# Performance work log

Measured on AMD Instinct MI355X. Metric: run time of the kernel, lower is better.

Reference implementation:

```python
import jax, jax.numpy as jnp
import numpy as np

B, T, IN, H = 1024, 200, 128, 128

def _linear_params(key, out_dim, in_dim):
    kw, kb = jax.random.split(key)
    bound = 1.0 / np.sqrt(in_dim)
    w = jax.random.uniform(kw, (out_dim, in_dim), jnp.float32, -bound, bound)
    b = jax.random.uniform(kb, (out_dim,), jnp.float32, -bound, bound)
    return w, b

def setup_inputs() -> dict:
    key = jax.random.key(0)
    ks = jax.random.split(key, 10)
    targets = jax.random.normal(ks[0], (B, T, IN), jnp.float32)
    history_states = jax.random.normal(ks[1], (B, T, H), jnp.float32)
    W_w, W_b = _linear_params(ks[2], H, IN)
    xu_w, xu_b = _linear_params(ks[3], H, H)
    hu_w, hu_b = _linear_params(ks[4], H, H)
    xr_w, xr_b = _linear_params(ks[5], H, H)
    hr_w, hr_b = _linear_params(ks[6], H, H)
    xg_w, xg_b = _linear_params(ks[7], H, H)
    hg_w, hg_b = _linear_params(ks[8], H, H)
    ln2_w, ln2_b = _linear_params(ks[9], H, IN + H)
    return dict(targets=targets, history_states=history_states,
                W_w=W_w, W_b=W_b, xu_w=xu_w, xu_b=xu_b, hu_w=hu_w, hu_b=hu_b,
                xr_w=xr_w, xr_b=xr_b, hr_w=hr_w, hr_b=hr_b,
                xg_w=xg_w, xg_b=xg_b, hg_w=hg_w, hg_b=hg_b,
                ln2_w=ln2_w, ln2_b=ln2_b)

def reference(targets, history_states, W_w, W_b, xu_w, xu_b, hu_w, hu_b,
              xr_w, xr_b, hr_w, hr_b, xg_w, xg_b, hg_w, hg_b, ln2_w, ln2_b):
    # attention weights: softmax over time of <W(targets), history>
    aw = jnp.einsum('bti,hi->bth', targets, W_w) + W_b            # [B,T,H]
    att = jax.nn.softmax(jnp.sum(aw * history_states, -1, keepdims=True), axis=1)  # [B,T,1]

    # precompute input-side projections as big GEMMs (same math as per-step Linear)
    xu = jnp.einsum('bth,oh->bto', history_states, xu_w) + xu_b   # [B,T,H]
    xr = jnp.einsum('bth,oh->bto', history_states, xr_w) + xr_b
    xg = jnp.einsum('bth,oh->bto', history_states, xg_w) + xg_b

    def step(h, xs):
        xu_t, xr_t, xg_t, a_t = xs                                 # [B,H],[B,H],[B,H],[B,1]
        u = jax.nn.sigmoid(xu_t + h @ hu_w.T + hu_b) * a_t
        r = jax.nn.sigmoid(xr_t + h @ hr_w.T + hr_b)
        g = jnp.tanh(xg_t + r * (h @ hg_w.T + hg_b))
        h = (1.0 - u) * h + u * g
        return h, None

    h0 = jnp.zeros((targets.shape[0], hu_w.shape[0]), targets.dtype)
    # scan over time: move T to leading axis
    xs = (jnp.swapaxes(xu, 0, 1), jnp.swapaxes(xr, 0, 1),
          jnp.swapaxes(xg, 0, 1), jnp.swapaxes(att, 0, 1))
    h, _ = jax.lax.scan(step, h0, xs)

    out = jnp.concatenate([h, targets[:, 0]], axis=-1) @ ln2_w.T + ln2_b
    return out
```

## Files before the change

kernel.cpp:

```cpp
#include <hip/hip_runtime.h>

#define B_ 1024
#define T_ 200
#define H_ 128
#define TSTR (T_ + 4)

typedef __attribute__((ext_vector_type(8))) short short8;
typedef __attribute__((ext_vector_type(4))) float f32x4;

#define MFMA(a, b, c) __builtin_amdgcn_mfma_f32_16x16x32_bf16((a), (b), (c), 0, 0, 0)

static __device__ __forceinline__ short f2bf(float f) {
  unsigned u = __float_as_uint(f);
  u += 0x7fffu + ((u >> 16) & 1u);
  return (short)(u >> 16);
}
static __device__ __forceinline__ float bf2f(short s) {
  return __uint_as_float(((unsigned)(unsigned short)s) << 16);
}
static __device__ __forceinline__ unsigned pack2bf_rne(float a, float b) {
  unsigned ua = __float_as_uint(a);
  ua += 0x7fffu + ((ua >> 16) & 1u);
  unsigned ub = __float_as_uint(b);
  ub += 0x7fffu + ((ub >> 16) & 1u);
  return (ua >> 16) | (ub & 0xFFFF0000u);
}
static __device__ __forceinline__ unsigned pack2bf_trunc(float a, float b) {
  return (__float_as_uint(a) >> 16) | (__float_as_uint(b) & 0xFFFF0000u);
}
static __device__ __forceinline__ float rcp_f(float x) { return __builtin_amdgcn_rcpf(x); }
static __device__ __forceinline__ float exp2_f(float x) { return __builtin_amdgcn_exp2f(x); }
static __device__ __forceinline__ void ck_barrier() {
  asm volatile("s_waitcnt lgkmcnt(0)\n\ts_barrier" ::: "memory");
}

__global__ __launch_bounds__(512, 1) void proj_scores_kernel(
    const float* __restrict__ tgt, const float* __restrict__ hist,
    const float* __restrict__ Ww, const float* __restrict__ Wb,
    float* __restrict__ scores, short* __restrict__ histbf) {
  const int tc = blockIdx.x, bb = blockIdx.y;
  const int nt = (tc == 12) ? 8 : 16;
  const int t0 = tc * 16;
  const int tid = threadIdx.x;
  const int lane = tid & 63, w = tid >> 6;
  const int n = lane & 15, q = lane >> 4;

  __shared__ short tgt_hi[2][16 * 128];
  __shared__ short tgt_lo[2][16 * 128];
  __shared__ float hist_f[2][16 * 132];
  __shared__ float sp[2][16 * 8];

  short8 whi[4], wlo[4];
  f32x4 wb4;
  {
    const int o = w * 16 + n;
#pragma unroll
    for (int ks = 0; ks < 4; ++ks) {
      const float* p = Ww + o * H_ + ks * 32 + q * 8;
      short8 h, l;
#pragma unroll
      for (int j = 0; j < 8; ++j) {
        float f = p[j];
        short hv = f2bf(f);
        h[j] = hv;
        l[j] = f2bf(f - bf2f(hv));
      }
      whi[ks] = h;
      wlo[ks] = l;
    }
    wb4 = *(const f32x4*)(Wb + w * 16 + q * 4);
  }

  const int sm = tid >> 5, cs = tid & 31;
  const int g = cs >> 1, half = cs & 1;
  const int spos16 = sm * 128 + ((g ^ (sm & 7)) * 8) + half * 4;
  const int sposf = sm * 132 + cs * 4;
  const size_t rowbase = ((size_t)(bb * 16 + sm) * T_) * H_ + cs * 4;

  const int cu = tid;
  const int cks = cu >> 7, crem = cu & 127, cwl = crem >> 1, chalf = crem & 1;
  const int crow = cwl & 15, ckb = cks * 32 + (cwl >> 4) * 8 + chalf * 4;

  float4 hv = *(const float4*)(hist + rowbase + (size_t)t0 * H_);
  float4 tv = *(const float4*)(tgt + rowbase + (size_t)t0 * H_);
  {
    *(float4*)&hist_f[0][sposf] = hv;
    uint2 hi, lo;
    hi.x = pack2bf_rne(tv.x, tv.y);
    hi.y = pack2bf_rne(tv.z, tv.w);
    lo.x = pack2bf_rne(tv.x - bf2f((short)(hi.x)), tv.y - bf2f((short)(hi.x >> 16)));
    lo.y = pack2bf_rne(tv.z - bf2f((short)(hi.y)), tv.w - bf2f((short)(hi.y >> 16)));
    *(uint2*)&tgt_hi[0][spos16] = hi;
    *(uint2*)&tgt_lo[0][spos16] = lo;
  }
  ck_barrier();

  for (int tl = 0; tl < nt; ++tl) {
    const int cur = tl & 1, nxt = cur ^ 1;
    const bool have_next = (tl + 1 < nt);
    if (have_next) {
      hv = *(const float4*)(hist + rowbase + (size_t)(t0 + tl + 1) * H_);
      tv = *(const float4*)(tgt + rowbase + (size_t)(t0 + tl + 1) * H_);
    }
    f32x4 s1 = {0, 0, 0, 0}, s2 = {0, 0, 0, 0}, s3 = {0, 0, 0, 0};
#pragma unroll
    for (int ks = 0; ks < 4; ++ks) {
      const int fp = n * 128 + ((ks * 4 + q) ^ (n & 7)) * 8;
      short8 ahi = *(short8*)&tgt_hi[cur][fp];
      short8 alo = *(short8*)&tgt_lo[cur][fp];
      s1 = MFMA(whi[ks], ahi, s1);
      s2 = MFMA(wlo[ks], ahi, s2);
      s3 = MFMA(whi[ks], alo, s3);
    }
    {
      f32x4 hv4 = *(const f32x4*)&hist_f[cur][n * 132 + w * 16 + q * 4];
      float v = (s1[0] + s2[0] + s3[0] + wb4[0]) * hv4[0];
      v += (s1[1] + s2[1] + s3[1] + wb4[1]) * hv4[1];
      v += (s1[2] + s2[2] + s3[2] + wb4[2]) * hv4[2];
      v += (s1[3] + s2[3] + s3[3] + wb4[3]) * hv4[3];
      v += __shfl_xor(v, 16);
      v += __shfl_xor(v, 32);
      if (lane < 16) sp[cur][n * 8 + w] = v;
    }
    if (histbf != nullptr) {
      const float* src = &hist_f[cur][crow * 132 + ckb];
      uint2 u;
      u.x = pack2bf_rne(src[0], src[1]);
      u.y = pack2bf_rne(src[2], src[3]);
      const size_t sb =
          (((size_t)(bb * TSTR + t0 + tl) * 4) + cks) * 512 + cwl * 8 + chalf * 4;
      *(uint2*)(histbf + sb) = u;
    }
    if (have_next) {
      *(float4*)&hist_f[nxt][sposf] = hv;
      uint2 hi, lo;
      hi.x = pack2bf_rne(tv.x, tv.y);
      hi.y = pack2bf_rne(tv.z, tv.w);
      lo.x = pack2bf_rne(tv.x - bf2f((short)(hi.x)), tv.y - bf2f((short)(hi.x >> 16)));
      lo.y = pack2bf_rne(tv.z - bf2f((short)(hi.y)), tv.w - bf2f((short)(hi.y >> 16)));
      *(uint2*)&tgt_hi[nxt][spos16] = hi;
      *(uint2*)&tgt_lo[nxt][spos16] = lo;
    }
    ck_barrier();
    if (tid < 16) {
      float s = 0.0f;
#pragma unroll
      for (int ww = 0; ww < 8; ++ww) s += sp[cur][tid * 8 + ww];
      scores[(size_t)(bb * 16 + tid) * T_ + (t0 + tl)] = s;
    }
  }
}

__global__ __launch_bounds__(256, 4) void softmax_kernel(float* __restrict__ att) {
  const int b = blockIdx.x, tid = threadIdx.x;
  const int lane = tid & 63, wave = tid >> 6;
  __shared__ float red[8];
  float v = (tid < T_) ? att[(size_t)b * T_ + tid] : -3.0e38f;
  float mx = v;
#pragma unroll
  for (int d = 1; d < 64; d <<= 1) mx = fmaxf(mx, __shfl_xor(mx, d));
  if (lane == 0) red[wave] = mx;
  __syncthreads();
  mx = fmaxf(fmaxf(red[0], red[1]), fmaxf(red[2], red[3]));
  float e = (tid < T_) ? __expf(v - mx) : 0.0f;
  float sm = e;
#pragma unroll
  for (int d = 1; d < 64; d <<= 1) sm += __shfl_xor(sm, d);
  if (lane == 0) red[4 + wave] = sm;
  __syncthreads();
  sm = red[4] + red[5] + red[6] + red[7];
  if (tid < T_) att[(size_t)b * T_ + tid] = e / sm;
}

template <bool DIRECT>
__global__ __launch_bounds__(512, 1) void scan3_kernel(
    const float* __restrict__ hist,
    const float* __restrict__ xu_w, const float* __restrict__ xu_b,
    const float* __restrict__ hu_w, const float* __restrict__ hu_b,
    const float* __restrict__ xr_w, const float* __restrict__ xr_b,
    const float* __restrict__ hr_w, const float* __restrict__ hr_b,
    const float* __restrict__ xg_w, const float* __restrict__ xg_b,
    const float* __restrict__ hg_w, const float* __restrict__ hg_b,
    const float* __restrict__ att, const short* __restrict__ histbf,
    float* __restrict__ h_out) {
  const int tid = threadIdx.x;
  const int lane = tid & 63, w = tid >> 6;
  const int n = lane & 15, q = lane >> 4;
  const int bb = blockIdx.x, r0 = bb * 16;
  const int o = w * 16 + n;
  const int ob = w * 16 + q * 4;

  constexpr float LOG2E = 1.4426950408889634f;

  __shared__ short hbuf[2][16 * 128];
  __shared__ short xbuf[2][16 * 128];

  short8 wf[6][4];
  {
    const float* Wm[6] = {xu_w, hu_w, xr_w, hr_w, xg_w, hg_w};
    const float Sc[6] = {LOG2E, LOG2E, LOG2E, LOG2E, 2.0f * LOG2E, 2.0f * LOG2E};
#pragma unroll
    for (int M = 0; M < 6; ++M)
#pragma unroll
      for (int ks = 0; ks < 4; ++ks) {
        const float* p = Wm[M] + o * H_ + ks * 32 + q * 8;
        short8 v;
#pragma unroll
        for (int j = 0; j < 8; ++j) v[j] = f2bf(p[j] * Sc[M]);
        wf[M][ks] = v;
      }
  }
  const f32x4 bu4 = (*(const f32x4*)(xu_b + ob) + *(const f32x4*)(hu_b + ob)) * LOG2E;
  const f32x4 br4 = (*(const f32x4*)(xr_b + ob) + *(const f32x4*)(hr_b + ob)) * LOG2E;
  const f32x4 bxg4 = *(const f32x4*)(xg_b + ob) * (2.0f * LOG2E);
  const f32x4 bhg4 = *(const f32x4*)(hg_b + ob) * (2.0f * LOG2E);

  for (int i = tid; i < 16 * 128; i += 512) hbuf[0][i] = 0;

  typedef union { uint4 u; short8 s; } frag_u;
  frag_u xp[2][4];
  const short* px = histbf + ((size_t)bb * TSTR * 4) * 512 + (size_t)lane * 8;
  const int sm = tid >> 5, cs = tid & 31;
  const int xpos = sm * 128 + (((cs >> 1) ^ (sm & 7)) * 8) + (cs & 1) * 4;
  const float* hrow = hist + ((size_t)(r0 + sm) * T_) * H_ + cs * 4;
  float4 xnext;

  f32x4 xq[2][3];

  if constexpr (DIRECT) {
    frag_u x0[4];
#pragma unroll
    for (int ks = 0; ks < 4; ++ks)
      x0[ks].u = *(const uint4*)(px + (size_t)(0 * 4 + ks) * 512);
#pragma unroll
    for (int ks = 0; ks < 4; ++ks)
      xp[1][ks].u = *(const uint4*)(px + (size_t)(1 * 4 + ks) * 512);
#pragma unroll
    for (int ks = 0; ks < 4; ++ks)
      xp[0][ks].u = *(const uint4*)(px + (size_t)(2 * 4 + ks) * 512);
    xq[0][0] = MFMA(wf[0][0], x0[0].s, bu4);
    xq[0][1] = MFMA(wf[2][0], x0[0].s, br4);
    xq[0][2] = MFMA(wf[4][0], x0[0].s, bxg4);
#pragma unroll
    for (int ks = 1; ks < 4; ++ks) {
      xq[0][0] = MFMA(wf[0][ks], x0[ks].s, xq[0][0]);
      xq[0][1] = MFMA(wf[2][ks], x0[ks].s, xq[0][1]);
      xq[0][2] = MFMA(wf[4][ks], x0[ks].s, xq[0][2]);
    }
  } else {
    float4 a = *(const float4*)hrow;
    uint2 u;
    u.x = pack2bf_rne(a.x, a.y);
    u.y = pack2bf_rne(a.z, a.w);
    *(uint2*)&xbuf[0][xpos] = u;
    xnext = *(const float4*)(hrow + H_);
  }

  const float* pa = att + (size_t)(r0 + n) * T_;
  f32x4 ab0 = *(const f32x4*)(pa + 0);
  f32x4 ab1 = *(const f32x4*)(pa + 4);

  float hreg[4] = {0.0f, 0.0f, 0.0f, 0.0f};
  const int wri = n * 128 + (((w * 2 + (q >> 1)) ^ (n & 7)) * 8) + (q & 1) * 4;
  ck_barrier();

  if constexpr (DIRECT) {
    const short* pxt = px + (size_t)12 * 512;
    for (int tb = 0; tb < T_; tb += 8) {
#pragma unroll
      for (int k = 0; k < 8; ++k) {
        const int t = tb + k;
        const int cur = k & 1, nxt = cur ^ 1;
        short8 ha[4];
#pragma unroll
        for (int ks = 0; ks < 4; ++ks)
          ha[ks] = *(short8*)&hbuf[cur][n * 128 + ((ks * 4 + q) ^ (n & 7)) * 8];

        f32x4 ahu = MFMA(wf[1][0], ha[0], xq[cur][0]);
        f32x4 ahr = MFMA(wf[3][0], ha[0], xq[cur][1]);
        f32x4 ahg = MFMA(wf[5][0], ha[0], bhg4);
#pragma unroll
        for (int ks = 1; ks < 4; ++ks) {
          ahu = MFMA(wf[1][ks], ha[ks], ahu);
          ahr = MFMA(wf[3][ks], ha[ks], ahr);
          ahg = MFMA(wf[5][ks], ha[ks], ahg);
        }

        {
          const short8 x0s = xp[nxt][0].s;
          xq[nxt][0] = MFMA(wf[0][0], x0s, bu4);
          xq[nxt][1] = MFMA(wf[2][0], x0s, br4);
          xq[nxt][2] = MFMA(wf[4][0], x0s, bxg4);
#pragma unroll
          for (int ks = 1; ks < 4; ++ks) {
            const short8 xs = xp[nxt][ks].s;
            xq[nxt][0] = MFMA(wf[0][ks], xs, xq[nxt][0]);
            xq[nxt][1] = MFMA(wf[2][ks], xs, xq[nxt][1]);
            xq[nxt][2] = MFMA(wf[4][ks], xs, xq[nxt][2]);
          }
        }
#pragma unroll
        for (int ks = 0; ks < 4; ++ks)
          xp[nxt][ks].u = *(const uint4*)(pxt + (size_t)(k * 4 + ks) * 512);

        const float at = ((k >> 2) & 1) ? ab1[k & 3] : ab0[k & 3];
        if (k == 3) ab0 = *(const f32x4*)(pa + ((t + 5 <= T_ - 4) ? t + 5 : T_ - 4));
        if (k == 7) ab1 = *(const f32x4*)(pa + ((t + 5 <= T_ - 4) ? t + 5 : T_ - 4));

        float hn[4];
#pragma unroll
        for (int r = 0; r < 4; ++r) {
          const float uu = at * rcp_f(1.0f + exp2_f(-ahu[r]));
          const float rr = rcp_f(1.0f + exp2_f(-ahr[r]));
          const float sg = xq[cur][2][r] + rr * ahg[r];
          const float g = 2.0f * rcp_f(1.0f + exp2_f(-sg)) - 1.0f;
          hn[r] = hreg[r] + uu * (g - hreg[r]);
          hreg[r] = hn[r];
        }

        uint2 up;
        up.x = pack2bf_trunc(hn[0], hn[1]);
        up.y = pack2bf_trunc(hn[2], hn[3]);
        *(uint2*)&hbuf[nxt][wri] = up;
        ck_barrier();
      }
      pxt += (size_t)8 * 4 * 512;
    }
  } else {
#pragma unroll 2
    for (int t = 0; t < T_; ++t) {
      const int cur = t & 1, nxt = cur ^ 1;
      short8 ha[4];
#pragma unroll
      for (int ks = 0; ks < 4; ++ks)
        ha[ks] = *(short8*)&hbuf[cur][n * 128 + ((ks * 4 + q) ^ (n & 7)) * 8];
      short8 xa[4];
#pragma unroll
      for (int ks = 0; ks < 4; ++ks)
        xa[ks] = *(short8*)&xbuf[cur][n * 128 + ((ks * 4 + q) ^ (n & 7)) * 8];
      f32x4 xu_a = MFMA(wf[0][0], xa[0], bu4);
      f32x4 xr_a = MFMA(wf[2][0], xa[0], br4);
      f32x4 xg_a = MFMA(wf[4][0], xa[0], bxg4);
#pragma unroll
      for (int ks = 1; ks < 4; ++ks) {
        xu_a = MFMA(wf[0][ks], xa[ks], xu_a);
        xr_a = MFMA(wf[2][ks], xa[ks], xr_a);
        xg_a = MFMA(wf[4][ks], xa[ks], xg_a);
      }
      f32x4 ahu = MFMA(wf[1][0], ha[0], xu_a);
      f32x4 ahr = MFMA(wf[3][0], ha[0], xr_a);
      f32x4 ahg = MFMA(wf[5][0], ha[0], bhg4);
#pragma unroll
      for (int ks = 1; ks < 4; ++ks) {
        ahu = MFMA(wf[1][ks], ha[ks], ahu);
        ahr = MFMA(wf[3][ks], ha[ks], ahr);
        ahg = MFMA(wf[5][ks], ha[ks], ahg);
      }
      const int tp = (t + 2 < T_) ? t + 2 : T_ - 1;
      const float at = ((t >> 2) & 1) ? ab1[t & 3] : ab0[t & 3];
      if ((t & 7) == 3) ab0 = *(const f32x4*)(pa + ((t + 5 <= T_ - 4) ? t + 5 : T_ - 4));
      if ((t & 7) == 7) ab1 = *(const f32x4*)(pa + ((t + 5 <= T_ - 4) ? t + 5 : T_ - 4));
      float hn[4];
#pragma unroll
      for (int r = 0; r < 4; ++r) {
        const float uu = at * rcp_f(1.0f + exp2_f(-ahu[r]));
        const float rr = rcp_f(1.0f + exp2_f(-ahr[r]));
        const float sg = xg_a[r] + rr * ahg[r];
        const float g = 2.0f * rcp_f(1.0f + exp2_f(-sg)) - 1.0f;
        hn[r] = hreg[r] + uu * (g - hreg[r]);
        hreg[r] = hn[r];
      }
      uint2 up;
      up.x = pack2bf_trunc(hn[0], hn[1]);
      up.y = pack2bf_trunc(hn[2], hn[3]);
      *(uint2*)&hbuf[nxt][wri] = up;
      uint2 u;
      u.x = pack2bf_rne(xnext.x, xnext.y);
      u.y = pack2bf_rne(xnext.z, xnext.w);
      *(uint2*)&xbuf[nxt][xpos] = u;
      xnext = *(const float4*)(hrow + (size_t)tp * H_);
      ck_barrier();
    }
  }

  f32x4 hv = {hreg[0], hreg[1], hreg[2], hreg[3]};
  *(f32x4*)(h_out + (size_t)(r0 + n) * H_ + ob) = hv;
}

__global__ __launch_bounds__(256, 4) void final_kernel(
    const float* __restrict__ tgt, const float* __restrict__ hfin,
    const float* __restrict__ w, const float* __restrict__ bias,
    float* __restrict__ out) {
  const int b = blockIdx.x, tid = threadIdx.x;
  const int o = tid >> 1, half = tid & 1;
  const float* src = half ? (tgt + (size_t)b * (T_ * H_)) : (hfin + (size_t)b * H_);
  const float* wrow = w + o * 256 + half * 128;
  float acc = 0.0f;
#pragma unroll 8
  for (int k = 0; k < 128; k += 4) {
    float4 sv = *(const float4*)(src + k);
    float4 wv = *(const float4*)(wrow + k);
    acc += sv.x * wv.x + sv.y * wv.y + sv.z * wv.z + sv.w * wv.w;
  }
  acc += __shfl_xor(acc, 1);
  if (half == 0) out[(size_t)b * H_ + o] = acc + bias[o];
}

extern "C" void kernel_launch(void* const* d_in, const int* in_sizes, int n_in,
                              void* d_out, int out_size, void* d_ws, size_t ws_size,
                              hipStream_t stream) {
  const float* targets = (const float*)d_in[0];
  const float* history = (const float*)d_in[1];
  const float* W_w = (const float*)d_in[2];
  const float* W_b = (const float*)d_in[3];
  const float* xu_w = (const float*)d_in[4];
  const float* xu_b = (const float*)d_in[5];
  const float* hu_w = (const float*)d_in[6];
  const float* hu_b = (const float*)d_in[7];
  const float* xr_w = (const float*)d_in[8];
  const float* xr_b = (const float*)d_in[9];
  const float* hr_w = (const float*)d_in[10];
  const float* hr_b = (const float*)d_in[11];
  const float* xg_w = (const float*)d_in[12];
  const float* xg_b = (const float*)d_in[13];
  const float* hg_w = (const float*)d_in[14];
  const float* hg_b = (const float*)d_in[15];
  const float* ln2_w = (const float*)d_in[16];
  const float* ln2_b = (const float*)d_in[17];
  float* out = (float*)d_out;

  float* att = (float*)d_ws;
  float* hfin = att + (size_t)B_ * T_;
  const size_t fixed = (size_t)B_ * T_ * 4 + (size_t)B_ * H_ * 4;
  const size_t histbf_bytes = (size_t)64 * TSTR * 4 * 512 * 2;
  short* histbf = (ws_size >= fixed + histbf_bytes)
                      ? (short*)((char*)d_ws + fixed)
                      : nullptr;

  proj_scores_kernel<<<dim3(13, 64), dim3(512), 0, stream>>>(
      targets, history, W_w, W_b, att, histbf);
  softmax_kernel<<<dim3(B_), dim3(256), 0, stream>>>(att);
  if (histbf) {
    scan3_kernel<true><<<dim3(64), dim3(512), 0, stream>>>(
        history, xu_w, xu_b, hu_w, hu_b, xr_w, xr_b, hr_w, hr_b,
        xg_w, xg_b, hg_w, hg_b, att, histbf, hfin);
  } else {
    scan3_kernel<false><<<dim3(64), dim3(512), 0, stream>>>(
        history, xu_w, xu_b, hu_w, hu_b, xr_w, xr_b, hr_w, hr_b,
        xg_w, xg_b, hg_w, hg_b, att, histbf, hfin);
  }
  final_kernel<<<dim3(B_), dim3(256), 0, stream>>>(targets, hfin, ln2_w, ln2_b, out);
}
```

Measured before the change: 445.9 us.

## Fuse softmax into scan kernel, batch final GEMV rows, reorder recurrent MFMAs

Drops the separate softmax launch. Each scan block now computes the softmax over time for its 16 batch rows into LDS at startup, and the per-step attention values are read from LDS instead of global memory. The final projection kernel handles four batch rows per block so each weight load is reused four times. Inside the step loop, the input-projection MFMAs for the next step are issued before the recurrent MFMAs, and the bf16 truncation pack uses a single perm instruction. The trade-off is extra LDS per scan block and some redundant startup work in the serial scan kernel.

```diff
diff --git a/kernel.cpp b/kernel.cpp
--- a/kernel.cpp
+++ b/kernel.cpp
@@ -26,7 +26,7 @@
   return (ua >> 16) | (ub & 0xFFFF0000u);
 }
 static __device__ __forceinline__ unsigned pack2bf_trunc(float a, float b) {
-  return (__float_as_uint(a) >> 16) | (__float_as_uint(b) & 0xFFFF0000u);
+  return __builtin_amdgcn_perm(__float_as_uint(b), __float_as_uint(a), 0x07060302u);
 }
 static __device__ __forceinline__ float rcp_f(float x) { return __builtin_amdgcn_rcpf(x); }
 static __device__ __forceinline__ float exp2_f(float x) { return __builtin_amdgcn_exp2f(x); }
@@ -151,27 +151,6 @@
   }
 }
 
-__global__ __launch_bounds__(256, 4) void softmax_kernel(float* __restrict__ att) {
-  const int b = blockIdx.x, tid = threadIdx.x;
-  const int lane = tid & 63, wave = tid >> 6;
-  __shared__ float red[8];
-  float v = (tid < T_) ? att[(size_t)b * T_ + tid] : -3.0e38f;
-  float mx = v;
-#pragma unroll
-  for (int d = 1; d < 64; d <<= 1) mx = fmaxf(mx, __shfl_xor(mx, d));
-  if (lane == 0) red[wave] = mx;
-  __syncthreads();
-  mx = fmaxf(fmaxf(red[0], red[1]), fmaxf(red[2], red[3]));
-  float e = (tid < T_) ? __expf(v - mx) : 0.0f;
-  float sm = e;
-#pragma unroll
-  for (int d = 1; d < 64; d <<= 1) sm += __shfl_xor(sm, d);
-  if (lane == 0) red[4 + wave] = sm;
-  __syncthreads();
-  sm = red[4] + red[5] + red[6] + red[7];
-  if (tid < T_) att[(size_t)b * T_ + tid] = e / sm;
-}
-
 template <bool DIRECT>
 __global__ __launch_bounds__(512, 1) void scan3_kernel(
     const float* __restrict__ hist,
@@ -181,7 +160,7 @@
     const float* __restrict__ hr_w, const float* __restrict__ hr_b,
     const float* __restrict__ xg_w, const float* __restrict__ xg_b,
     const float* __restrict__ hg_w, const float* __restrict__ hg_b,
-    const float* __restrict__ att, const short* __restrict__ histbf,
+    const float* __restrict__ att_g, const short* __restrict__ histbf,
     float* __restrict__ h_out) {
   const int tid = threadIdx.x;
   const int lane = tid & 63, w = tid >> 6;
@@ -194,6 +173,7 @@
 
   __shared__ short hbuf[2][16 * 128];
   __shared__ short xbuf[2][16 * 128];
+  __shared__ float att_lds[16 * 204];
 
   short8 wf[6][4];
   {
@@ -217,12 +197,41 @@
 
   for (int i = tid; i < 16 * 128; i += 512) hbuf[0][i] = 0;
 
+  {
+    const int row = tid >> 5, idx = tid & 31;
+    const float* srow = att_g + (size_t)(r0 + row) * T_;
+    float v[7];
+    float mx = -3.0e38f;
+#pragma unroll
+    for (int i = 0; i < 7; ++i) {
+      const int t = idx + i * 32;
+      v[i] = (t < T_) ? srow[t] : -3.0e38f;
+      mx = fmaxf(mx, v[i]);
+    }
+#pragma unroll
+    for (int d = 1; d < 32; d <<= 1) mx = fmaxf(mx, __shfl_xor(mx, d));
+    float sm = 0.0f;
+#pragma unroll
+    for (int i = 0; i < 7; ++i) {
+      v[i] = exp2_f((v[i] - mx) * LOG2E);
+      sm += v[i];
+    }
+#pragma unroll
+    for (int d = 1; d < 32; d <<= 1) sm += __shfl_xor(sm, d);
+    const float rs = rcp_f(sm);
+#pragma unroll
+    for (int i = 0; i < 7; ++i) {
+      const int t = idx + i * 32;
+      if (t < T_) att_lds[row * 204 + t] = v[i] * rs;
+    }
+  }
+
   typedef union { uint4 u; short8 s; } frag_u;
   frag_u xp[2][4];
   const short* px = histbf + ((size_t)bb * TSTR * 4) * 512 + (size_t)lane * 8;
-  const int sm = tid >> 5, cs = tid & 31;
-  const int xpos = sm * 128 + (((cs >> 1) ^ (sm & 7)) * 8) + (cs & 1) * 4;
-  const float* hrow = hist + ((size_t)(r0 + sm) * T_) * H_ + cs * 4;
+  const int sm_ = tid >> 5, cs = tid & 31;
+  const int xpos = sm_ * 128 + (((cs >> 1) ^ (sm_ & 7)) * 8) + (cs & 1) * 4;
+  const float* hrow = hist + ((size_t)(r0 + sm_) * T_) * H_ + cs * 4;
   float4 xnext;
 
   f32x4 xq[2][3];
@@ -256,13 +265,13 @@
     xnext = *(const float4*)(hrow + H_);
   }
 
-  const float* pa = att + (size_t)(r0 + n) * T_;
-  f32x4 ab0 = *(const f32x4*)(pa + 0);
-  f32x4 ab1 = *(const f32x4*)(pa + 4);
-
   float hreg[4] = {0.0f, 0.0f, 0.0f, 0.0f};
   const int wri = n * 128 + (((w * 2 + (q >> 1)) ^ (n & 7)) * 8) + (q & 1) * 4;
   ck_barrier();
+
+  const float* paL = &att_lds[n * 204];
+  f32x4 ab0 = *(const f32x4*)(paL + 0);
+  f32x4 ab1 = *(const f32x4*)(paL + 4);
 
   if constexpr (DIRECT) {
     const short* pxt = px + (size_t)12 * 512;
@@ -275,16 +284,6 @@
 #pragma unroll
         for (int ks = 0; ks < 4; ++ks)
           ha[ks] = *(short8*)&hbuf[cur][n * 128 + ((ks * 4 + q) ^ (n & 7)) * 8];
-
-        f32x4 ahu = MFMA(wf[1][0], ha[0], xq[cur][0]);
-        f32x4 ahr = MFMA(wf[3][0], ha[0], xq[cur][1]);
-        f32x4 ahg = MFMA(wf[5][0], ha[0], bhg4);
-#pragma unroll
-        for (int ks = 1; ks < 4; ++ks) {
-          ahu = MFMA(wf[1][ks], ha[ks], ahu);
-          ahr = MFMA(wf[3][ks], ha[ks], ahr);
-          ahg = MFMA(wf[5][ks], ha[ks], ahg);
-        }
 
         {
           const short8 x0s = xp[nxt][0].s;
@@ -299,13 +298,24 @@
             xq[nxt][2] = MFMA(wf[4][ks], xs, xq[nxt][2]);
           }
         }
+
+        f32x4 ahu = MFMA(wf[1][0], ha[0], xq[cur][0]);
+        f32x4 ahr = MFMA(wf[3][0], ha[0], xq[cur][1]);
+        f32x4 ahg = MFMA(wf[5][0], ha[0], bhg4);
+#pragma unroll
+        for (int ks = 1; ks < 4; ++ks) {
+          ahu = MFMA(wf[1][ks], ha[ks], ahu);
+          ahr = MFMA(wf[3][ks], ha[ks], ahr);
+          ahg = MFMA(wf[5][ks], ha[ks], ahg);
+        }
+
 #pragma unroll
         for (int ks = 0; ks < 4; ++ks)
           xp[nxt][ks].u = *(const uint4*)(pxt + (size_t)(k * 4 + ks) * 512);
 
         const float at = ((k >> 2) & 1) ? ab1[k & 3] : ab0[k & 3];
-        if (k == 3) ab0 = *(const f32x4*)(pa + ((t + 5 <= T_ - 4) ? t + 5 : T_ - 4));
-        if (k == 7) ab1 = *(const f32x4*)(pa + ((t + 5 <= T_ - 4) ? t + 5 : T_ - 4));
+        if (k == 3) ab0 = *(const f32x4*)(paL + ((t + 5 <= T_ - 4) ? t + 5 : T_ - 4));
+        if (k == 7) ab1 = *(const f32x4*)(paL + ((t + 5 <= T_ - 4) ? t + 5 : T_ - 4));
 
         float hn[4];
 #pragma unroll
@@ -358,8 +368,8 @@
       }
       const int tp = (t + 2 < T_) ? t + 2 : T_ - 1;
       const float at = ((t >> 2) & 1) ? ab1[t & 3] : ab0[t & 3];
-      if ((t & 7) == 3) ab0 = *(const f32x4*)(pa + ((t + 5 <= T_ - 4) ? t + 5 : T_ - 4));
-      if ((t & 7) == 7) ab1 = *(const f32x4*)(pa + ((t + 5 <= T_ - 4) ? t + 5 : T_ - 4));
+      if ((t & 7) == 3) ab0 = *(const f32x4*)(paL + ((t + 5 <= T_ - 4) ? t + 5 : T_ - 4));
+      if ((t & 7) == 7) ab1 = *(const f32x4*)(paL + ((t + 5 <= T_ - 4) ? t + 5 : T_ - 4));
       float hn[4];
 #pragma unroll
       for (int r = 0; r < 4; ++r) {
@@ -391,19 +401,38 @@
     const float* __restrict__ tgt, const float* __restrict__ hfin,
     const float* __restrict__ w, const float* __restrict__ bias,
     float* __restrict__ out) {
-  const int b = blockIdx.x, tid = threadIdx.x;
+  const int b4 = blockIdx.x * 4, tid = threadIdx.x;
   const int o = tid >> 1, half = tid & 1;
-  const float* src = half ? (tgt + (size_t)b * (T_ * H_)) : (hfin + (size_t)b * H_);
   const float* wrow = w + o * 256 + half * 128;
-  float acc = 0.0f;
+  const float* s0 = half ? (tgt + (size_t)(b4 + 0) * (T_ * H_)) : (hfin + (size_t)(b4 + 0) * H_);
+  const float* s1 = half ? (tgt + (size_t)(b4 + 1) * (T_ * H_)) : (hfin + (size_t)(b4 + 1) * H_);
+  const float* s2 = half ? (tgt + (size_t)(b4 + 2) * (T_ * H_)) : (hfin + (size_t)(b4 + 2) * H_);
+  const float* s3 = half ? (tgt + (size_t)(b4 + 3) * (T_ * H_)) : (hfin + (size_t)(b4 + 3) * H_);
+  float a0 = 0.0f, a1 = 0.0f, a2 = 0.0f, a3 = 0.0f;
 #pragma unroll 8
   for (int k = 0; k < 128; k += 4) {
-    float4 sv = *(const float4*)(src + k);
-    float4 wv = *(const float4*)(wrow + k);
-    acc += sv.x * wv.x + sv.y * wv.y + sv.z * wv.z + sv.w * wv.w;
-  }
-  acc += __shfl_xor(acc, 1);
-  if (half == 0) out[(size_t)b * H_ + o] = acc + bias[o];
+    const float4 wv = *(const float4*)(wrow + k);
+    float4 v;
+    v = *(const float4*)(s0 + k);
+    a0 += v.x * wv.x + v.y * wv.y + v.z * wv.z + v.w * wv.w;
+    v = *(const float4*)(s1 + k);
+    a1 += v.x * wv.x + v.y * wv.y + v.z * wv.z + v.w * wv.w;
+    v = *(const float4*)(s2 + k);
+    a2 += v.x * wv.x + v.y * wv.y + v.z * wv.z + v.w * wv.w;
+    v = *(const float4*)(s3 + k);
+    a3 += v.x * wv.x + v.y * wv.y + v.z * wv.z + v.w * wv.w;
+  }
+  a0 += __shfl_xor(a0, 1);
+  a1 += __shfl_xor(a1, 1);
+  a2 += __shfl_xor(a2, 1);
+  a3 += __shfl_xor(a3, 1);
+  if (half == 0) {
+    const float bo = bias[o];
+    out[(size_t)(b4 + 0) * H_ + o] = a0 + bo;
+    out[(size_t)(b4 + 1) * H_ + o] = a1 + bo;
+    out[(size_t)(b4 + 2) * H_ + o] = a2 + bo;
+    out[(size_t)(b4 + 3) * H_ + o] = a3 + bo;
+  }
 }
 
 extern "C" void kernel_launch(void* const* d_in, const int* in_sizes, int n_in,
@@ -439,7 +468,6 @@
 
   proj_scores_kernel<<<dim3(13, 64), dim3(512), 0, stream>>>(
       targets, history, W_w, W_b, att, histbf);
-  softmax_kernel<<<dim3(B_), dim3(256), 0, stream>>>(att);
   if (histbf) {
     scan3_kernel<true><<<dim3(64), dim3(512), 0, stream>>>(
         history, xu_w, xu_b, hu_w, hu_b, xr_w, xr_b, hr_w, hr_b,
@@ -449,5 +477,5 @@
         history, xu_w, xu_b, hu_w, hu_b, xr_w, xr_b, hr_w, hr_b,
         xg_w, xg_b, hg_w, hg_b, att, histbf, hfin);
   }
-  final_kernel<<<dim3(B_), dim3(256), 0, stream>>>(targets, hfin, ln2_w, ln2_b, out);
-}
+  final_kernel<<<dim3(B_ / 4), dim3(256), 0, stream>>>(targets, hfin, ln2_w, ln2_b, out);
+}
```

New measurement: 434.1 us. -2.6%, faster.
